# Performance work log

Hardware: AMD Instinct MI355X
Metric: run time of the kernel (lower is better)

Reference implementation:

```python
import jax, jax.numpy as jnp
import numpy as np

B, T, V, E, H = 1024, 256, 90, 8, 256


def setup_inputs() -> dict:
    key = jax.random.key(0)
    ks = jax.random.split(key, 40)
    rn = lambda k, shape: jax.random.normal(k, shape, dtype=jnp.float32) * 0.05
    inp = {}
    inp["input_seq"] = jax.random.randint(ks[0], (B, T), 0, V, dtype=jnp.int32)
    inp["emb"] = rn(ks[1], (V, E)).at[0].set(0.0)  # padding_idx=0
    i = 2
    for name, din in [("g1", E), ("g2", H), ("l1", E), ("l2", H)]:
        inp[name + "_Wih"] = rn(ks[i], (4 * H, din)); i += 1
        inp[name + "_Whh"] = rn(ks[i], (4 * H, H)); i += 1
        inp[name + "_bih"] = rn(ks[i], (4 * H,)); i += 1
        inp[name + "_bhh"] = rn(ks[i], (4 * H,)); i += 1
    for name in ["p1", "p2"]:
        inp[name + "_W1"] = rn(ks[i], (2 * H, E + 4 * H)); i += 1
        inp[name + "_b1"] = rn(ks[i], (2 * H,)); i += 1
        inp[name + "_W2"] = rn(ks[i], (H, 2 * H)); i += 1
        inp[name + "_b2"] = rn(ks[i], (H,)); i += 1
        inp[name + "_W3"] = rn(ks[i], (2, H)); i += 1
        inp[name + "_b3"] = rn(ks[i], (2,)); i += 1
    inp["gfc_W"] = rn(ks[i], (V, H)); i += 1
    inp["gfc_b"] = rn(ks[i], (V,)); i += 1
    inp["lfc_W"] = rn(ks[i], (V, H)); i += 1
    inp["lfc_b"] = rn(ks[i], (V,))
    return inp


def _cell(x, h, c, Wih, Whh, bih, bhh):
    # PyTorch LSTMCell: gate order i, f, g, o
    g = x @ Wih.T + h @ Whh.T + (bih + bhh)
    i, f, gg, o = jnp.split(g, 4, axis=-1)
    c = jax.nn.sigmoid(f) * c + jax.nn.sigmoid(i) * jnp.tanh(gg)
    return jax.nn.sigmoid(o) * jnp.tanh(c), c


def _mlp(x, W1, b1, W2, b2, W3, b3):
    h = jax.nn.relu(x @ W1.T + b1)
    h = jax.nn.relu(h @ W2.T + b2)
    return h @ W3.T + b3


def _forward(input_seq, emb,
             g1_Wih, g1_Whh, g1_bih, g1_bhh, g2_Wih, g2_Whh, g2_bih, g2_bhh,
             l1_Wih, l1_Whh, l1_bih, l1_bhh, l2_Wih, l2_Whh, l2_bih, l2_bhh,
             p1_W1, p1_b1, p1_W2, p1_b2, p1_W3, p1_b3,
             p2_W1, p2_b1, p2_W2, p2_b2, p2_W3, p2_b3,
             gfc_W, gfc_b, lfc_W, lfc_b):
    Bn = input_seq.shape[0]
    embeds = emb[input_seq]  # [B, T, E]
    z = jnp.zeros((Bn, H), dtype=emb.dtype)

    def step(carry, e):
        gh1, gc1, gh2, gc2, lh1, lc1, lh2, lc2 = carry
        gh1, gc1 = _cell(e, gh1, gc1, g1_Wih, g1_Whh, g1_bih, g1_bhh)
        lh1, lc1 = _cell(e, lh1, lc1, l1_Wih, l1_Whh, l1_bih, l1_bhh)
        p = jax.nn.softmax(_mlp(jnp.concatenate([e, gh1, gc1, lh1, lc1], 1),
                                p1_W1, p1_b1, p1_W2, p1_b2, p1_W3, p1_b3), axis=1)
        # bmm([B,1,2],[B,2,H]) == p0*local + p1*global
        gh1 = p[:, 0:1] * lh1 + p[:, 1:2] * gh1
        gc1 = p[:, 0:1] * lc1 + p[:, 1:2] * gc1
        gh2, gc2 = _cell(gh1, gh2, gc2, g2_Wih, g2_Whh, g2_bih, g2_bhh)
        lh2, lc2 = _cell(lh1, lh2, lc2, l2_Wih, l2_Whh, l2_bih, l2_bhh)
        p = jax.nn.softmax(_mlp(jnp.concatenate([e, gh2, gc2, lh2, lc2], 1),
                                p2_W1, p2_b1, p2_W2, p2_b2, p2_W3, p2_b3), axis=1)
        gh2 = p[:, 0:1] * lh2 + p[:, 1:2] * gh2
        gc2 = p[:, 0:1] * lc2 + p[:, 1:2] * gc2
        return (gh1, gc1, gh2, gc2, lh1, lc1, lh2, lc2), gh2

    _, hs = jax.lax.scan(step, (z, z, z, z, z, z, z, z), jnp.swapaxes(embeds, 0, 1))
    hs = jnp.swapaxes(hs, 0, 1)  # [B, T, H]
    out = 0.5 * (hs @ gfc_W.T + gfc_b) + 0.5 * (hs @ lfc_W.T + lfc_b)
    return jnp.swapaxes(out, 1, 2)  # [B, V, T]


def reference(input_seq, emb,
              g1_Wih, g1_Whh, g1_bih, g1_bhh, g2_Wih, g2_Whh, g2_bih, g2_bhh,
              l1_Wih, l1_Whh, l1_bih, l1_bhh, l2_Wih, l2_Whh, l2_bih, l2_bhh,
              p1_W1, p1_b1, p1_W2, p1_b2, p1_W3, p1_b3,
              p2_W1, p2_b1, p2_W2, p2_b2, p2_W3, p2_b3,
              gfc_W, gfc_b, lfc_W, lfc_b):
    return _forward(input_seq, emb,
                    g1_Wih, g1_Whh, g1_bih, g1_bhh, g2_Wih, g2_Whh, g2_bih, g2_bhh,
                    l1_Wih, l1_Whh, l1_bih, l1_bhh, l2_Wih, l2_Whh, l2_bih, l2_bhh,
                    p1_W1, p1_b1, p1_W2, p1_b2, p1_W3, p1_b3,
                    p2_W1, p2_b1, p2_W2, p2_b2, p2_W3, p2_b3,
                    gfc_W, gfc_b, lfc_W, lfc_b)
```

## Files before the change

kernel.cpp:

```cpp
#include <hip/hip_runtime.h>

#define B_ 1024
#define T_ 256
#define V_ 90
#define H_ 256
#define NTHR 512
#define NBLK 256
#define S_ ((size_t)B_*H_)

typedef unsigned short u16;
typedef __attribute__((ext_vector_type(8))) _Float16 f16x8;
typedef __attribute__((ext_vector_type(4))) _Float16 f16x4;
typedef __attribute__((ext_vector_type(4))) float f32x4;

constexpr size_t OFF_GH1C  = 0;
constexpr size_t OFF_GC1C  = OFF_GH1C + S_;
constexpr size_t OFF_GH1P  = OFF_GC1C + S_;
constexpr size_t OFF_GC1P  = OFF_GH1P + S_;
constexpr size_t OFF_LH1   = OFF_GC1P + S_;
constexpr size_t OFF_LC1   = OFF_LH1 + 2*S_;
constexpr size_t OFF_GH2C  = OFF_LC1 + 2*S_;
constexpr size_t OFF_GC2C  = OFF_GH2C + S_;
constexpr size_t OFF_GH2P  = OFF_GC2C + S_;
constexpr size_t OFF_GC2P  = OFF_GH2P + S_;
constexpr size_t OFF_LH2   = OFF_GC2P + S_;
constexpr size_t OFF_LC2   = OFF_LH2 + 2*S_;
constexpr size_t OFF_M1H   = OFF_LC2 + 2*S_;
constexpr size_t OFF_M2H   = OFF_M1H + (size_t)B_*512/2;
constexpr size_t OFF_OSTG  = OFF_M2H + (size_t)B_*512/2;
constexpr size_t OFF_EX    = OFF_OSTG + (size_t)B_*16*90;
constexpr size_t OFF_WG1PK = OFF_EX + 2*B_*8;
constexpr size_t OFF_WE1   = OFF_WG1PK + 256*2048/2;
constexpr size_t OFF_BG1   = OFF_WE1 + 8*2048;
constexpr size_t OFF_WL2PK = OFF_BG1 + 2048;
constexpr size_t OFF_BL2   = OFF_WL2PK + 512*1024/2;
constexpr size_t OFF_WG2PK = OFF_BL2 + 1024;
constexpr size_t OFF_BG2   = OFF_WG2PK + 512*1024/2;
constexpr size_t OFF_WP1PK = OFF_BG2 + 1024;
constexpr size_t OFF_WEP1  = OFF_WP1PK + 1024*512/2;
constexpr size_t OFF_WP2PK = OFF_WEP1 + 8*512;
constexpr size_t OFF_WEP2  = OFF_WP2PK + 1024*512/2;
constexpr size_t OFF_WB1   = OFF_WEP2 + 8*512;
constexpr size_t OFF_WB2   = OFF_WB1 + 512*256/2;
constexpr size_t OFF_WOUT  = OFF_WB2 + 512*256/2;
constexpr size_t OFF_BOUT  = OFF_WOUT + 256*96;
constexpr size_t OFF_BAR   = OFF_BOUT + 128;
constexpr size_t WS_FLOATS = OFF_BAR + 8192;

struct InP {
  const int*   seq;
  const float* emb;
  const float *g1_Wih,*g1_Whh,*g1_bih,*g1_bhh;
  const float *g2_Wih,*g2_Whh,*g2_bih,*g2_bhh;
  const float *l1_Wih,*l1_Whh,*l1_bih,*l1_bhh;
  const float *l2_Wih,*l2_Whh,*l2_bih,*l2_bhh;
  const float *p1_W1,*p1_b1,*p1_W2,*p1_b2,*p1_W3,*p1_b3;
  const float *p2_W1,*p2_b1,*p2_W2,*p2_b2,*p2_W3,*p2_b3;
  const float *gfc_W,*gfc_b,*lfc_W,*lfc_b;
};

__device__ __forceinline__ float sig_(float x)  { return 1.f/(1.f+__expf(-x)); }
__device__ __forceinline__ float tanh_(float x) { return 1.f - 2.f/(__expf(2.f*x)+1.f); }
__device__ __forceinline__ u16 f2h(float v) {
  _Float16 h = (_Float16)v; return __builtin_bit_cast(unsigned short, h);
}

__device__ __forceinline__ unsigned ld_flag(const unsigned* p) {
  unsigned v;
  asm volatile("global_load_dword %0, %1, off sc1\n\ts_waitcnt vmcnt(0)"
               : "=v"(v) : "v"(p) : "memory");
  return v;
}
__device__ __forceinline__ void st_flag(unsigned* p, unsigned v) {
  asm volatile("global_store_dword %0, %1, off sc1\n\ts_waitcnt vmcnt(0)"
               :: "v"(p), "v"(v) : "memory");
}

__device__ __forceinline__ void gbar_x(unsigned* arr, int slot, unsigned ep)
{
  __syncthreads();
  if (threadIdx.x == 0) st_flag(&arr[slot*16], ep);
  if (threadIdx.x < 32) {
    int cap = 0;
    for (;;) {
      unsigned v = ld_flag(&arr[threadIdx.x*16]);
      if (v >= ep) break;
      __builtin_amdgcn_s_sleep(1);
      if (++cap > 200000) break;
    }
  }
  __syncthreads();
  asm volatile("buffer_inv sc0" ::: "memory");
}

__device__ __forceinline__ void gl_lds16(const void* g, void* l) {
  __builtin_amdgcn_global_load_lds(
      (const __attribute__((address_space(1))) unsigned int*)g,
      (__attribute__((address_space(3))) unsigned int*)l, 16, 0, 2);
}
__device__ __forceinline__ void dma64(const u16* src) {
  extern __shared__ u16 dynB[];
  const int wv = threadIdx.x >> 6, lane = threadIdx.x & 63;
  const char* g = (const char*)src + lane*16;
  char* l = (char*)dynB;
#pragma unroll
  for (int j = 0; j < 8; ++j) {
    const int ofs = (wv*8 + j) * 1024;
    gl_lds16(g + ofs, l + ofs);
  }
}

template<int NCH, int NSEG, bool HASE, int TPW, class FE>
__device__ __forceinline__ void mm_lds(
    const float* s0, const float* s1_, const float* s2_, const float* s3_,
    const float* WeP, int ldwe, const float* ex,
    int rows0, int ct0, FE fe)
{
  extern __shared__ u16 dynB[];
  const int tid = threadIdx.x, lane = tid & 63, wr = tid >> 6;
  const int row = rows0 + wr*16 + (lane & 15);
  const int kq  = (lane >> 4) << 3;

  f32x4 acc[TPW];
#pragma unroll
  for (int t = 0; t < TPW; ++t) acc[t] = (f32x4){0,0,0,0};

  float4 alo[4], ahi[4];
  auto ldA = [&](int c, float4& lo, float4& hi) {
    const int k0 = c * 32;
    const float* S;
    if (NSEG == 1) S = s0;
    else if (NSEG == 2) S = (k0 < 256) ? s0 : s1_;
    else S = (k0 < 256) ? s0 : (k0 < 512) ? s1_ : (k0 < 768) ? s2_ : s3_;
    const float* p = &S[(size_t)row*H_ + (k0 & 255) + kq];
    lo = *(const float4*)p; hi = *(const float4*)(p + 4);
  };
  auto comp = [&](int c, const float4& lo, const float4& hi) {
    float av[8] = {lo.x,lo.y,lo.z,lo.w,hi.x,hi.y,hi.z,hi.w};
    f16x8 a;
#pragma unroll
    for (int j = 0; j < 8; ++j) a[j] = (_Float16)av[j];
#pragma unroll
    for (int t = 0; t < TPW; ++t) {
      f16x8 b = *(const f16x8*)(dynB + (size_t)(c*TPW + t)*512 + lane*8);
      acc[t] = __builtin_amdgcn_mfma_f32_16x16x32_f16(a, b, acc[t], 0, 0, 0);
    }
  };

#pragma unroll
  for (int c = 0; c < 4; ++c) ldA(c, alo[c], ahi[c]);
#pragma unroll
  for (int c = 0; c < NCH; ++c) {
    comp(c, alo[c & 3], ahi[c & 3]);
    if (c + 4 < NCH) ldA(c + 4, alo[c & 3], ahi[c & 3]);
  }

  if (HASE) {
#pragma unroll
    for (int t = 0; t < TPW; ++t) {
      const int colL = ct0 + t*16 + (lane & 15);
      float w[8];
#pragma unroll
      for (int j = 0; j < 8; ++j) w[j] = WeP[j*ldwe + colL];
#pragma unroll
      for (int m = 0; m < 4; ++m) {
        const int rr = rows0 + wr*16 + ((lane >> 4) << 2) + m;
        float s = 0.f;
#pragma unroll
        for (int j = 0; j < 8; ++j) s = __builtin_fmaf(ex[rr*8 + j], w[j], s);
        acc[t][m] += s;
      }
    }
  }
  fe(wr, lane, acc);
}

template<int TPW>
struct GateEpiM {
  const float* cin; float* ho; float* co; const float* bias_pk;
  int rows0; int ct0;
  __device__ void operator()(int wr, int lane, f32x4 (&acc)[TPW]) const {
    const int rbase = rows0 + wr*16 + ((lane >> 4) << 2);
#pragma unroll
    for (int gi = 0; gi < TPW/4; ++gi) {
      const int cb = ct0 + gi*64;
      const int h = (((cb & 1023) >> 6) << 4) + (lane & 15);
      float b[4];
#pragma unroll
      for (int t = 0; t < 4; ++t) b[t] = bias_pk[cb + t*16 + (lane & 15)];
#pragma unroll
      for (int m = 0; m < 4; ++m) {
        const size_t ix = (size_t)(rbase + m)*H_ + h;
        float gI = sig_(acc[gi*4+0][m] + b[0]);
        float gF = sig_(acc[gi*4+1][m] + b[1]);
        float gG = tanh_(acc[gi*4+2][m] + b[2]);
        float gO = sig_(acc[gi*4+3][m] + b[3]);
        float cn = gF*cin[ix] + gI*gG;
        ho[ix] = gO*tanh_(cn); co[ix] = cn;
      }
    }
  }
};

struct MlpEpiH {
  u16* dst; const float* b1; int rows0; int ct0;
  __device__ void operator()(int wr, int lane, f32x4 (&acc)[2]) const {
    const int rbase = rows0 + wr*16 + ((lane >> 4) << 2);
#pragma unroll
    for (int t = 0; t < 2; ++t) {
      const int c = ct0 + t*16 + (lane & 15);
      const float bb = b1[c];
#pragma unroll
      for (int m = 0; m < 4; ++m)
        dst[(size_t)(rbase + m)*512 + c] = f2h(fmaxf(acc[t][m] + bb, 0.f));
    }
  }
};

__device__ __forceinline__ void stage_F2(
    int rowbase,
    const u16* M, const u16* WBpk, const float* b2,
    const float* W3, const float* b3,
    const float* lh, const float* lc,
    const float* ghp, const float* gcp,
    float* ghc, float* gcc)
{
  const int w = threadIdx.x >> 6, lane = threadIdx.x & 63;
  const int r0 = rowbase + w*2;
  const u16* a0 = M + (size_t)r0*512;
  const u16* a1 = a0 + 512;
  float m0[4] = {0.f,0.f,0.f,0.f}, m1[4] = {0.f,0.f,0.f,0.f};
  for (int k0 = 0; k0 < 512; k0 += 4) {
    f16x4 x0 = *(const f16x4*)&a0[k0];
    f16x4 x1 = *(const f16x4*)&a1[k0];
#pragma unroll
    for (int j = 0; j < 4; ++j) {
      f16x4 wv = *(const f16x4*)&WBpk[(size_t)(k0+j)*256 + lane*4];
      float w0 = (float)wv[0], w1 = (float)wv[1], w2 = (float)wv[2], w3v = (float)wv[3];
      float xv0 = (float)x0[j], xv1 = (float)x1[j];
      m0[0] = __builtin_fmaf(xv0, w0, m0[0]);
      m0[1] = __builtin_fmaf(xv0, w1, m0[1]);
      m0[2] = __builtin_fmaf(xv0, w2, m0[2]);
      m0[3] = __builtin_fmaf(xv0, w3v, m0[3]);
      m1[0] = __builtin_fmaf(xv1, w0, m1[0]);
      m1[1] = __builtin_fmaf(xv1, w1, m1[1]);
      m1[2] = __builtin_fmaf(xv1, w2, m1[2]);
      m1[3] = __builtin_fmaf(xv1, w3v, m1[3]);
    }
  }
  float4 b = *(const float4*)&b2[lane*4];
  float bb2[4] = {b.x,b.y,b.z,b.w};
#pragma unroll
  for (int j = 0; j < 4; ++j) {
    m0[j] = fmaxf(m0[j]+bb2[j], 0.f);
    m1[j] = fmaxf(m1[j]+bb2[j], 0.f);
  }
  float4 w30 = *(const float4*)&W3[lane*4];
  float4 w31 = *(const float4*)&W3[256 + lane*4];
  float w0v[4] = {w30.x,w30.y,w30.z,w30.w};
  float w1v[4] = {w31.x,w31.y,w31.z,w31.w};
  float d00=0.f, d01=0.f, d10=0.f, d11=0.f;
#pragma unroll
  for (int j = 0; j < 4; ++j) {
    d00 = __builtin_fmaf(m0[j], w0v[j], d00);
    d01 = __builtin_fmaf(m0[j], w1v[j], d01);
    d10 = __builtin_fmaf(m1[j], w0v[j], d10);
    d11 = __builtin_fmaf(m1[j], w1v[j], d11);
  }
#pragma unroll
  for (int off = 32; off; off >>= 1) {
    d00 += __shfl_xor(d00, off, 64); d01 += __shfl_xor(d01, off, 64);
    d10 += __shfl_xor(d10, off, 64); d11 += __shfl_xor(d11, off, 64);
  }
  d00 += b3[0]; d01 += b3[1]; d10 += b3[0]; d11 += b3[1];
  float mxa = fmaxf(d00, d01), mxb = fmaxf(d10, d11);
  float e00 = __expf(d00-mxa), e01 = __expf(d01-mxa);
  float e10 = __expf(d10-mxb), e11 = __expf(d11-mxb);
  float ia = 1.f/(e00+e01), ib = 1.f/(e10+e11);
  float p0a = e00*ia, p1a = e01*ia;
  float p0b = e10*ib, p1b = e11*ib;
#pragma unroll
  for (int rr = 0; rr < 2; ++rr) {
    const float p0 = rr ? p0b : p0a, p1 = rr ? p1b : p1a;
    const size_t ix = (size_t)(r0+rr)*H_ + lane*4;
    float4 lv = *(const float4*)&lh[ix];
    float4 gv = *(const float4*)&ghp[ix];
    float4 o;
    o.x = p0*lv.x + p1*gv.x; o.y = p0*lv.y + p1*gv.y;
    o.z = p0*lv.z + p1*gv.z; o.w = p0*lv.w + p1*gv.w;
    *(float4*)&ghc[ix] = o;
    lv = *(const float4*)&lc[ix];
    gv = *(const float4*)&gcp[ix];
    o.x = p0*lv.x + p1*gv.x; o.y = p0*lv.y + p1*gv.y;
    o.z = p0*lv.z + p1*gv.z; o.w = p0*lv.w + p1*gv.w;
    *(float4*)&gcc[ix] = o;
  }
}

__device__ __forceinline__ void stage_OUTS(
    const float* gh2c, const float* WOUT, const float* BOUT,
    float* ostg, int rbase, int tt)
{
  const int w = threadIdx.x >> 6, lane = threadIdx.x & 63;
  const bool two = lane < (V_ - 64);
#pragma unroll
  for (int rr = 0; rr < 2; ++rr) {
    const int r = rbase + w*2 + rr;
    const float* arow = gh2c + (size_t)r * H_;
    float acc0 = 0.f, acc1 = 0.f;
    for (int k0 = 0; k0 < 256; k0 += 4) {
      float4 a4 = *(const float4*)&arow[k0];
      float av[4] = {a4.x, a4.y, a4.z, a4.w};
#pragma unroll
      for (int j = 0; j < 4; ++j) {
        const float* wr_ = &WOUT[(size_t)(k0+j)*96];
        acc0 = __builtin_fmaf(av[j], wr_[lane], acc0);
        if (two) acc1 = __builtin_fmaf(av[j], wr_[64+lane], acc1);
      }
    }
    float* dst = &ostg[((size_t)r*16 + (tt & 15))*90];
    if (lane < 64) dst[lane] = acc0 + BOUT[lane];
    if (two) dst[64+lane] = acc1 + BOUT[64+lane];
  }
}

__device__ __forceinline__ void flush_out(
    const float* ostg, float* out, int rbase, int tb0)
{
  for (int i = threadIdx.x; i < 16*90; i += NTHR) {
    const int rr = i / 90, v = i - rr*90;
    const int r = rbase + rr;
    const float* src = &ostg[((size_t)r*16)*90 + v];
    float tmp[16];
#pragma unroll
    for (int tb = 0; tb < 16; ++tb) tmp[tb] = src[tb*90];
    float* dst = &out[((size_t)r*V_ + v)*T_ + tb0];
#pragma unroll
    for (int q = 0; q < 4; ++q)
      ((float4*)dst)[q] = make_float4(tmp[q*4], tmp[q*4+1], tmp[q*4+2], tmp[q*4+3]);
  }
}

__global__ void k_setup(InP in, float* __restrict__ ws)
{
  const size_t nthr = (size_t)gridDim.x * blockDim.x;
  const size_t t0 = (size_t)blockIdx.x * blockDim.x + threadIdx.x;

  for (size_t i = t0; i < 16*S_; i += nthr) ws[i] = 0.f;
  for (size_t i = t0; i < 8192; i += nthr) ((unsigned*)(ws + OFF_BAR))[i] = 0u;

  for (size_t i = t0; i < (size_t)B_*8; i += nthr) {
    int r = (int)(i >> 3), j = (int)(i & 7);
    ws[OFF_EX + i] = in.emb[(size_t)in.seq[(size_t)r*T_]*8 + j];
  }

  {
    u16* dst = (u16*)(ws + OFF_WG1PK);
    for (size_t i = t0; i < (size_t)16*8*8*512; i += nthr) {
      int e = (int)(i & 7), lane = (int)((i >> 3) & 63);
      int tile = (int)((i >> 9) & 7), ck = (int)((i >> 12) & 7), blk = (int)(i >> 15);
      int col = blk*128 + tile*16 + (lane & 15);
      int k = ck*32 + ((lane >> 4) << 3) + e;
      int cell = col >> 10, q = col & 1023;
      int h = ((q >> 6) << 4) + (q & 15), g = (q >> 4) & 3, R = g*256 + h;
      dst[i] = f2h((cell ? in.l1_Whh : in.g1_Whh)[(size_t)R*256 + k]);
    }
  }
  for (size_t i = t0; i < (size_t)8*2048; i += nthr) {
    int j = (int)(i >> 11), p = (int)(i & 2047);
    int cell = p >> 10, q = p & 1023;
    int h = ((q >> 6) << 4) + (q & 15), g = (q >> 4) & 3, R = g*256 + h;
    ws[OFF_WE1 + (size_t)j*2048 + p] = (cell ? in.l1_Wih : in.g1_Wih)[(size_t)R*8 + j];
  }
  for (size_t i = t0; i < 2048; i += nthr) {
    int p = (int)i, cell = p >> 10, q = p & 1023;
    int h = ((q >> 6) << 4) + (q & 15), g = (q >> 4) & 3, R = g*256 + h;
    ws[OFF_BG1 + i] = cell ? (in.l1_bih[R] + in.l1_bhh[R]) : (in.g1_bih[R] + in.g1_bhh[R]);
  }

  for (int which = 0; which < 2; ++which) {
    u16* dst = (u16*)(ws + (which ? OFF_WG2PK : OFF_WL2PK));
    const float* Wih = which ? in.g2_Wih : in.l2_Wih;
    const float* Whh = which ? in.g2_Whh : in.l2_Whh;
    for (size_t i = t0; i < (size_t)16*16*4*512; i += nthr) {
      int e = (int)(i & 7), lane = (int)((i >> 3) & 63);
      int tile = (int)((i >> 9) & 3), ck = (int)((i >> 11) & 15), blk = (int)(i >> 15);
      int col = blk*64 + tile*16 + (lane & 15);
      int k = ck*32 + ((lane >> 4) << 3) + e;
      int h = ((col >> 6) << 4) + (col & 15), g = (col >> 4) & 3, R = g*256 + h;
      float w = (k < 256) ? Wih[(size_t)R*256 + k] : Whh[(size_t)R*256 + (k-256)];
      dst[i] = f2h(w);
    }
  }
  for (size_t i = t0; i < 2*1024; i += nthr) {
    int which = (int)(i >> 10), p = (int)(i & 1023);
    int h = ((p >> 6) << 4) + (p & 15), g = (p >> 4) & 3, R = g*256 + h;
    float v = which ? (in.g2_bih[R] + in.g2_bhh[R]) : (in.l2_bih[R] + in.l2_bhh[R]);
    ws[(which ? OFF_BG2 : OFF_BL2) + p] = v;
  }

  for (int which = 0; which < 2; ++which) {
    u16* dst = (u16*)(ws + (which ? OFF_WP2PK : OFF_WP1PK));
    const float* W = which ? in.p2_W1 : in.p1_W1;
    for (size_t i = t0; i < (size_t)16*32*2*512; i += nthr) {
      int e = (int)(i & 7), lane = (int)((i >> 3) & 63);
      int tile = (int)((i >> 9) & 1), ck = (int)((i >> 10) & 31), blk = (int)(i >> 15);
      int col = blk*32 + tile*16 + (lane & 15);
      int k = ck*32 + ((lane >> 4) << 3) + e;
      dst[i] = f2h(W[(size_t)col*1032 + 8 + k]);
    }
  }
  for (size_t i = t0; i < (size_t)2*8*512; i += nthr) {
    int which = (int)(i / (8*512));
    int idx = (int)(i - (size_t)which*8*512);
    int j = idx >> 9, p = idx & 511;
    const float* W = which ? in.p2_W1 : in.p1_W1;
    ws[(which ? OFF_WEP2 : OFF_WEP1) + (size_t)j*512 + p] = W[(size_t)p*1032 + j];
  }

  for (size_t i = t0; i < (size_t)2*512*256; i += nthr) {
    int which = (int)(i / (512*256));
    int idx = (int)(i - (size_t)which*512*256);
    int k = idx >> 8, n = idx & 255;
    const float* W = which ? in.p2_W2 : in.p1_W2;
    ((u16*)(ws + (which ? OFF_WB2 : OFF_WB1)))[idx] = f2h(W[(size_t)n*512 + k]);
  }
  for (size_t i = t0; i < (size_t)256*96; i += nthr) {
    int k = (int)(i / 96), c = (int)(i - (size_t)k*96);
    float v = 0.f;
    if (c < V_) v = 0.5f*(in.gfc_W[(size_t)c*256 + k] + in.lfc_W[(size_t)c*256 + k]);
    ws[OFF_WOUT + i] = v;
  }
  for (size_t i = t0; i < 96; i += nthr)
    ws[OFF_BOUT + i] = (i < V_) ? 0.5f*(in.gfc_b[i] + in.lfc_b[i]) : 0.f;
}

__global__ __launch_bounds__(NTHR) void k_main(InP in, float* ws, float* __restrict__ out)
{
  __shared__ __attribute__((aligned(16))) volatile float s_pad[6144];
  __shared__ unsigned s_slot;

  float* GH1C = ws + OFF_GH1C;  float* GC1C = ws + OFF_GC1C;
  float* GH1P = ws + OFF_GH1P;  float* GC1P = ws + OFF_GC1P;
  float* LH1  = ws + OFF_LH1;   float* LC1  = ws + OFF_LC1;
  float* GH2C = ws + OFF_GH2C;  float* GC2C = ws + OFF_GC2C;
  float* GH2P = ws + OFF_GH2P;  float* GC2P = ws + OFF_GC2P;
  float* LH2  = ws + OFF_LH2;   float* LC2  = ws + OFF_LC2;
  u16*   M1H  = (u16*)(ws + OFF_M1H);
  u16*   M2H  = (u16*)(ws + OFF_M2H);
  float* OSTG = ws + OFF_OSTG;
  float* EXB  = ws + OFF_EX;
  const u16* WG1PK = (const u16*)(ws + OFF_WG1PK);
  const u16* WL2PK = (const u16*)(ws + OFF_WL2PK);
  const u16* WG2PK = (const u16*)(ws + OFF_WG2PK);
  const u16* WP1PK = (const u16*)(ws + OFF_WP1PK);
  const u16* WP2PK = (const u16*)(ws + OFF_WP2PK);
  const u16* WB1PK = (const u16*)(ws + OFF_WB1);
  const u16* WB2PK = (const u16*)(ws + OFF_WB2);
  const float* WE1  = ws + OFF_WE1;  const float* BG1P = ws + OFF_BG1;
  const float* BL2P = ws + OFF_BL2;  const float* BG2P = ws + OFF_BG2;
  const float* WEP1 = ws + OFF_WEP1; const float* WEP2 = ws + OFF_WEP2;
  const float* WOUT = ws + OFF_WOUT; const float* BOUT = ws + OFF_BOUT;

  unsigned xcc;
  asm volatile("s_getreg_b32 %0, hwreg(HW_REG_XCC_ID)" : "=s"(xcc));
  xcc &= 7u;
  unsigned* barx = ((unsigned*)(ws + OFF_BAR)) + xcc*1024;
  unsigned* arr  = barx;
  unsigned* reg  = barx + 544;
  if (threadIdx.x == 0) {
    s_slot = __hip_atomic_fetch_add(reg, 1u, __ATOMIC_RELAXED, __HIP_MEMORY_SCOPE_AGENT);
    s_pad[0] = (float)s_slot;
  }
  __syncthreads();
  const int slot  = (int)(s_slot & 31u);
  const int rows0 = (int)xcc * 128;
  const int s2 = slot & 15;
  unsigned ep = 0;

  if (slot < 16) dma64(WG1PK + (size_t)slot*32768);
  else           dma64(WG2PK + (size_t)s2*32768);
  asm volatile("s_waitcnt vmcnt(0)" ::: "memory");
  __syncthreads();

  for (int n = 0; n <= T_; ++n) {
    const int sel = n & 1;
    const float* ex  = EXB + sel*(B_*8);
    const float* exm = EXB + (sel^1)*(B_*8);
    float* lh1o = LH1 + sel*S_;   float* lh1n = LH1 + (sel^1)*S_;
    float* lc1o = LC1 + sel*S_;   float* lc1n = LC1 + (sel^1)*S_;
    float* lh2o = LH2 + sel*S_;   float* lh2n = LH2 + (sel^1)*S_;
    float* lc2o = LC2 + sel*S_;   float* lc2n = LC2 + (sel^1)*S_;

    if (slot < 16) {
      if (n < T_) {
        const int ct0 = slot*128;
        const int cell = slot >> 3;
        GateEpiM<8> epi{ cell ? lc1o : GC1C,
                         cell ? lh1n : GH1P,
                         cell ? lc1n : GC1P,
                         BG1P, rows0, ct0 };
        mm_lds<8,1,true,8>(cell ? lh1o : GH1C, nullptr, nullptr, nullptr,
                           WE1, 2048, ex, rows0, ct0, epi);
      }
    } else if (n >= 1) {
      const int ct0 = s2*64;
      GateEpiM<4> epi{ GC2C, GH2P, GC2P, BG2P, rows0, ct0 };
      mm_lds<16,2,false,4>(GH1C, GH2C, nullptr, nullptr,
                           nullptr, 0, nullptr, rows0, ct0, epi);
    }
    __syncthreads();
    {
      if (slot < 16) dma64(WP1PK + (size_t)s2*32768);
      else           dma64(WP2PK + (size_t)s2*32768);
    }
    gbar_x(arr, slot, ++ep);

    if (slot < 16) {
      if (n < T_) {
        const int ct0 = s2*32;
        MlpEpiH epi{ M1H, in.p1_b1, rows0, ct0 };
        mm_lds<32,4,true,2>(GH1P, GC1P, lh1n, lc1n,
                            WEP1, 512, ex, rows0, ct0, epi);
      }
    } else if (n >= 1) {
      const int ct0 = s2*32;
      MlpEpiH epi{ M2H, in.p2_b1, rows0, ct0 };
      mm_lds<32,4,true,2>(GH2P, GC2P, lh2o, lc2o,
                          WEP2, 512, exm, rows0, ct0, epi);
    }
    __syncthreads();
    if (n < T_) {
      if (slot < 16) dma64(WL2PK + (size_t)slot*32768);
      else           dma64(WG2PK + (size_t)s2*32768);
    }
    gbar_x(arr, slot, ++ep);

    if (slot < 16) {
      if (n < T_) {
        const int ct0 = slot*64;
        GateEpiM<4> epi{ lc2o, lh2n, lc2n, BL2P, rows0, ct0 };
        mm_lds<16,2,false,4>(lh1n, lh2o, nullptr, nullptr,
                             nullptr, 0, nullptr, rows0, ct0, epi);
      }
    } else if (slot < 24) {
      if (n < T_) {
        const int rb = rows0 + (slot-16)*16;
        stage_F2(rb, M1H, WB1PK, in.p1_b2, in.p1_W3, in.p1_b3,
                 lh1n, lc1n, GH1P, GC1P, GH1C, GC1C);
        if (n + 1 < T_ && threadIdx.x < 128) {
          const int r = rb + (threadIdx.x >> 3), j = threadIdx.x & 7;
          EXB[(sel^1)*(B_*8) + r*8 + j] =
              in.emb[(size_t)in.seq[(size_t)r*T_ + n + 1]*8 + j];
        }
      }
    } else {
      if (n >= 1) {
        const int rb = rows0 + (slot-24)*16;
        stage_F2(rb, M2H, WB2PK, in.p2_b2, in.p2_W3, in.p2_b3,
                 lh2o, lc2o, GH2P, GC2P, GH2C, GC2C);
        __syncthreads();
        stage_OUTS(GH2C, WOUT, BOUT, OSTG, rb, n-1);
        if (((n-1) & 15) == 15) {
          __syncthreads();
          flush_out(OSTG, out, rb, n-16);
        }
      }
    }
    __syncthreads();
    if (n < T_ - 1) {
      if (slot < 16) dma64(WG1PK + (size_t)slot*32768);
    }
    gbar_x(arr, slot, ++ep);
  }
}

extern "C" void kernel_launch(void* const* d_in, const int* in_sizes, int n_in,
                              void* d_out, int out_size, void* d_ws, size_t ws_size,
                              hipStream_t stream)
{
  if (ws_size < WS_FLOATS * sizeof(float)) return;

  InP in;
  in.seq    = (const int*)  d_in[0];
  in.emb    = (const float*)d_in[1];
  in.g1_Wih = (const float*)d_in[2];  in.g1_Whh = (const float*)d_in[3];
  in.g1_bih = (const float*)d_in[4];  in.g1_bhh = (const float*)d_in[5];
  in.g2_Wih = (const float*)d_in[6];  in.g2_Whh = (const float*)d_in[7];
  in.g2_bih = (const float*)d_in[8];  in.g2_bhh = (const float*)d_in[9];
  in.l1_Wih = (const float*)d_in[10]; in.l1_Whh = (const float*)d_in[11];
  in.l1_bih = (const float*)d_in[12]; in.l1_bhh = (const float*)d_in[13];
  in.l2_Wih = (const float*)d_in[14]; in.l2_Whh = (const float*)d_in[15];
  in.l2_bih = (const float*)d_in[16]; in.l2_bhh = (const float*)d_in[17];
  in.p1_W1  = (const float*)d_in[18]; in.p1_b1  = (const float*)d_in[19];
  in.p1_W2  = (const float*)d_in[20]; in.p1_b2  = (const float*)d_in[21];
  in.p1_W3  = (const float*)d_in[22]; in.p1_b3  = (const float*)d_in[23];
  in.p2_W1  = (const float*)d_in[24]; in.p2_b1  = (const float*)d_in[25];
  in.p2_W2  = (const float*)d_in[26]; in.p2_b2  = (const float*)d_in[27];
  in.p2_W3  = (const float*)d_in[28]; in.p2_b3  = (const float*)d_in[29];
  in.gfc_W  = (const float*)d_in[30]; in.gfc_b  = (const float*)d_in[31];
  in.lfc_W  = (const float*)d_in[32]; in.lfc_b  = (const float*)d_in[33];

  float* ws  = (float*)d_ws;
  float* out = (float*)d_out;

  k_setup<<<512, 256, 0, stream>>>(in, ws);
  k_main <<<NBLK, NTHR, 65536, stream>>>(in, ws, out);
}
```

Before: 57.61 ms.

## Double-buffer LDS weight tiles and store hidden states in fp16

```diff
diff --git a/kernel.cpp b/kernel.cpp
--- a/kernel.cpp
+++ b/kernel.cpp
@@ -7,6 +7,7 @@
 #define NTHR 512
 #define NBLK 256
 #define S_ ((size_t)B_*H_)
+#define HS_ (S_/2)
 
 typedef unsigned short u16;
 typedef __attribute__((ext_vector_type(8))) _Float16 f16x8;
@@ -14,17 +15,21 @@
 typedef __attribute__((ext_vector_type(4))) float f32x4;
 
 constexpr size_t OFF_GH1C  = 0;
-constexpr size_t OFF_GC1C  = OFF_GH1C + S_;
-constexpr size_t OFF_GH1P  = OFF_GC1C + S_;
-constexpr size_t OFF_GC1P  = OFF_GH1P + S_;
-constexpr size_t OFF_LH1   = OFF_GC1P + S_;
-constexpr size_t OFF_LC1   = OFF_LH1 + 2*S_;
-constexpr size_t OFF_GH2C  = OFF_LC1 + 2*S_;
-constexpr size_t OFF_GC2C  = OFF_GH2C + S_;
-constexpr size_t OFF_GH2P  = OFF_GC2C + S_;
-constexpr size_t OFF_GC2P  = OFF_GH2P + S_;
-constexpr size_t OFF_LH2   = OFF_GC2P + S_;
-constexpr size_t OFF_LC2   = OFF_LH2 + 2*S_;
+constexpr size_t OFF_GH1P  = OFF_GH1C + HS_;
+constexpr size_t OFF_LH1   = OFF_GH1P + HS_;
+constexpr size_t OFF_GH2C  = OFF_LH1 + 2*HS_;
+constexpr size_t OFF_GH2P  = OFF_GH2C + HS_;
+constexpr size_t OFF_LH2   = OFF_GH2P + HS_;
+constexpr size_t OFF_GC1PH = OFF_LH2 + 2*HS_;
+constexpr size_t OFF_LC1H  = OFF_GC1PH + HS_;
+constexpr size_t OFF_GC2PH = OFF_LC1H + 2*HS_;
+constexpr size_t OFF_LC2H  = OFF_GC2PH + HS_;
+constexpr size_t OFF_GC1C  = OFF_LC2H + 2*HS_;
+constexpr size_t OFF_GC1P  = OFF_GC1C + S_;
+constexpr size_t OFF_LC1   = OFF_GC1P + S_;
+constexpr size_t OFF_GC2C  = OFF_LC1 + 2*S_;
+constexpr size_t OFF_GC2P  = OFF_GC2C + S_;
+constexpr size_t OFF_LC2   = OFF_GC2P + S_;
 constexpr size_t OFF_M1H   = OFF_LC2 + 2*S_;
 constexpr size_t OFF_M2H   = OFF_M1H + (size_t)B_*512/2;
 constexpr size_t OFF_OSTG  = OFF_M2H + (size_t)B_*512/2;
@@ -98,11 +103,10 @@
       (const __attribute__((address_space(1))) unsigned int*)g,
       (__attribute__((address_space(3))) unsigned int*)l, 16, 0, 2);
 }
-__device__ __forceinline__ void dma64(const u16* src) {
-  extern __shared__ u16 dynB[];
+__device__ __forceinline__ void dma64(const u16* src, u16* dstbase) {
   const int wv = threadIdx.x >> 6, lane = threadIdx.x & 63;
   const char* g = (const char*)src + lane*16;
-  char* l = (char*)dynB;
+  char* l = (char*)dstbase;
 #pragma unroll
   for (int j = 0; j < 8; ++j) {
     const int ofs = (wv*8 + j) * 1024;
@@ -112,11 +116,11 @@
 
 template<int NCH, int NSEG, bool HASE, int TPW, class FE>
 __device__ __forceinline__ void mm_lds(
-    const float* s0, const float* s1_, const float* s2_, const float* s3_,
+    const u16* bufp,
+    const u16* s0, const u16* s1_, const u16* s2_, const u16* s3_,
     const float* WeP, int ldwe, const float* ex,
     int rows0, int ct0, FE fe)
 {
-  extern __shared__ u16 dynB[];
   const int tid = threadIdx.x, lane = tid & 63, wr = tid >> 6;
   const int row = rows0 + wr*16 + (lane & 15);
   const int kq  = (lane >> 4) << 3;
@@ -125,34 +129,28 @@
 #pragma unroll
   for (int t = 0; t < TPW; ++t) acc[t] = (f32x4){0,0,0,0};
 
-  float4 alo[4], ahi[4];
-  auto ldA = [&](int c, float4& lo, float4& hi) {
+  constexpr int DEP = (NCH < 8) ? NCH : 8;
+  f16x8 areg[DEP];
+  auto ldA = [&](int c) -> f16x8 {
     const int k0 = c * 32;
-    const float* S;
+    const u16* S;
     if (NSEG == 1) S = s0;
     else if (NSEG == 2) S = (k0 < 256) ? s0 : s1_;
     else S = (k0 < 256) ? s0 : (k0 < 512) ? s1_ : (k0 < 768) ? s2_ : s3_;
-    const float* p = &S[(size_t)row*H_ + (k0 & 255) + kq];
-    lo = *(const float4*)p; hi = *(const float4*)(p + 4);
+    return *(const f16x8*)&S[(size_t)row*H_ + (k0 & 255) + kq];
   };
-  auto comp = [&](int c, const float4& lo, const float4& hi) {
-    float av[8] = {lo.x,lo.y,lo.z,lo.w,hi.x,hi.y,hi.z,hi.w};
-    f16x8 a;
-#pragma unroll
-    for (int j = 0; j < 8; ++j) a[j] = (_Float16)av[j];
+
+#pragma unroll
+  for (int c = 0; c < DEP; ++c) areg[c] = ldA(c);
+#pragma unroll
+  for (int c = 0; c < NCH; ++c) {
+    f16x8 a = areg[c % DEP];
 #pragma unroll
     for (int t = 0; t < TPW; ++t) {
-      f16x8 b = *(const f16x8*)(dynB + (size_t)(c*TPW + t)*512 + lane*8);
+      f16x8 b = *(const f16x8*)(bufp + (size_t)(c*TPW + t)*512 + lane*8);
       acc[t] = __builtin_amdgcn_mfma_f32_16x16x32_f16(a, b, acc[t], 0, 0, 0);
     }
-  };
-
-#pragma unroll
-  for (int c = 0; c < 4; ++c) ldA(c, alo[c], ahi[c]);
-#pragma unroll
-  for (int c = 0; c < NCH; ++c) {
-    comp(c, alo[c & 3], ahi[c & 3]);
-    if (c + 4 < NCH) ldA(c + 4, alo[c & 3], ahi[c & 3]);
+    if (c + DEP < NCH) areg[c % DEP] = ldA(c + DEP);
   }
 
   if (HASE) {
@@ -177,7 +175,7 @@
 
 template<int TPW>
 struct GateEpiM {
-  const float* cin; float* ho; float* co; const float* bias_pk;
+  const float* cin; u16* ho; float* co; u16* coh; const float* bias_pk;
   int rows0; int ct0;
   __device__ void operator()(int wr, int lane, f32x4 (&acc)[TPW]) const {
     const int rbase = rows0 + wr*16 + ((lane >> 4) << 2);
@@ -196,7 +194,9 @@
         float gG = tanh_(acc[gi*4+2][m] + b[2]);
         float gO = sig_(acc[gi*4+3][m] + b[3]);
         float cn = gF*cin[ix] + gI*gG;
-        ho[ix] = gO*tanh_(cn); co[ix] = cn;
+        ho[ix] = f2h(gO*tanh_(cn));
+        co[ix] = cn;
+        coh[ix] = f2h(cn);
       }
     }
   }
@@ -221,9 +221,9 @@
     int rowbase,
     const u16* M, const u16* WBpk, const float* b2,
     const float* W3, const float* b3,
-    const float* lh, const float* lc,
-    const float* ghp, const float* gcp,
-    float* ghc, float* gcc)
+    const u16* lh, const float* lc,
+    const u16* ghp, const float* gcp,
+    u16* ghc, float* gcc)
 {
   const int w = threadIdx.x >> 6, lane = threadIdx.x & 63;
   const int r0 = rowbase + w*2;
@@ -283,22 +283,24 @@
   for (int rr = 0; rr < 2; ++rr) {
     const float p0 = rr ? p0b : p0a, p1 = rr ? p1b : p1a;
     const size_t ix = (size_t)(r0+rr)*H_ + lane*4;
-    float4 lv = *(const float4*)&lh[ix];
-    float4 gv = *(const float4*)&ghp[ix];
-    float4 o;
-    o.x = p0*lv.x + p1*gv.x; o.y = p0*lv.y + p1*gv.y;
-    o.z = p0*lv.z + p1*gv.z; o.w = p0*lv.w + p1*gv.w;
-    *(float4*)&ghc[ix] = o;
-    lv = *(const float4*)&lc[ix];
-    gv = *(const float4*)&gcp[ix];
-    o.x = p0*lv.x + p1*gv.x; o.y = p0*lv.y + p1*gv.y;
-    o.z = p0*lv.z + p1*gv.z; o.w = p0*lv.w + p1*gv.w;
-    *(float4*)&gcc[ix] = o;
+    f16x4 lv = *(const f16x4*)&lh[ix];
+    f16x4 gv = *(const f16x4*)&ghp[ix];
+    f16x4 oh;
+#pragma unroll
+    for (int j = 0; j < 4; ++j)
+      oh[j] = (_Float16)(p0*(float)lv[j] + p1*(float)gv[j]);
+    *(f16x4*)&ghc[ix] = oh;
+    float4 lcv = *(const float4*)&lc[ix];
+    float4 gcv = *(const float4*)&gcp[ix];
+    float4 oc;
+    oc.x = p0*lcv.x + p1*gcv.x; oc.y = p0*lcv.y + p1*gcv.y;
+    oc.z = p0*lcv.z + p1*gcv.z; oc.w = p0*lcv.w + p1*gcv.w;
+    *(float4*)&gcc[ix] = oc;
   }
 }
 
 __device__ __forceinline__ void stage_OUTS(
-    const float* gh2c, const float* WOUT, const float* BOUT,
+    const u16* gh2c, const float* WOUT, const float* BOUT,
     float* ostg, int rbase, int tt)
 {
   const int w = threadIdx.x >> 6, lane = threadIdx.x & 63;
@@ -306,20 +308,20 @@
 #pragma unroll
   for (int rr = 0; rr < 2; ++rr) {
     const int r = rbase + w*2 + rr;
-    const float* arow = gh2c + (size_t)r * H_;
+    const u16* arow = gh2c + (size_t)r * H_;
     float acc0 = 0.f, acc1 = 0.f;
-    for (int k0 = 0; k0 < 256; k0 += 4) {
-      float4 a4 = *(const float4*)&arow[k0];
-      float av[4] = {a4.x, a4.y, a4.z, a4.w};
-#pragma unroll
-      for (int j = 0; j < 4; ++j) {
+    for (int k0 = 0; k0 < 256; k0 += 8) {
+      f16x8 a8 = *(const f16x8*)&arow[k0];
+#pragma unroll
+      for (int j = 0; j < 8; ++j) {
+        const float av = (float)a8[j];
         const float* wr_ = &WOUT[(size_t)(k0+j)*96];
-        acc0 = __builtin_fmaf(av[j], wr_[lane], acc0);
-        if (two) acc1 = __builtin_fmaf(av[j], wr_[64+lane], acc1);
+        acc0 = __builtin_fmaf(av, wr_[lane], acc0);
+        if (two) acc1 = __builtin_fmaf(av, wr_[64+lane], acc1);
       }
     }
     float* dst = &ostg[((size_t)r*16 + (tt & 15))*90];
-    if (lane < 64) dst[lane] = acc0 + BOUT[lane];
+    dst[lane] = acc0 + BOUT[lane];
     if (two) dst[64+lane] = acc1 + BOUT[64+lane];
   }
 }
@@ -346,7 +348,7 @@
   const size_t nthr = (size_t)gridDim.x * blockDim.x;
   const size_t t0 = (size_t)blockIdx.x * blockDim.x + threadIdx.x;
 
-  for (size_t i = t0; i < 16*S_; i += nthr) ws[i] = 0.f;
+  for (size_t i = t0; i < OFF_M1H; i += nthr) ws[i] = 0.f;
   for (size_t i = t0; i < 8192; i += nthr) ((unsigned*)(ws + OFF_BAR))[i] = 0u;
 
   for (size_t i = t0; i < (size_t)B_*8; i += nthr) {
@@ -437,15 +439,24 @@
 
 __global__ __launch_bounds__(NTHR) void k_main(InP in, float* ws, float* __restrict__ out)
 {
-  __shared__ __attribute__((aligned(16))) volatile float s_pad[6144];
+  __shared__ __attribute__((aligned(16))) u16 sB0[32768];
+  extern __shared__ u16 dynB[];
   __shared__ unsigned s_slot;
 
-  float* GH1C = ws + OFF_GH1C;  float* GC1C = ws + OFF_GC1C;
-  float* GH1P = ws + OFF_GH1P;  float* GC1P = ws + OFF_GC1P;
-  float* LH1  = ws + OFF_LH1;   float* LC1  = ws + OFF_LC1;
-  float* GH2C = ws + OFF_GH2C;  float* GC2C = ws + OFF_GC2C;
-  float* GH2P = ws + OFF_GH2P;  float* GC2P = ws + OFF_GC2P;
-  float* LH2  = ws + OFF_LH2;   float* LC2  = ws + OFF_LC2;
+  u16*  GH1C = (u16*)(ws + OFF_GH1C);
+  u16*  GH1P = (u16*)(ws + OFF_GH1P);
+  u16*  LH1  = (u16*)(ws + OFF_LH1);
+  u16*  GH2C = (u16*)(ws + OFF_GH2C);
+  u16*  GH2P = (u16*)(ws + OFF_GH2P);
+  u16*  LH2  = (u16*)(ws + OFF_LH2);
+  u16*  GC1PH= (u16*)(ws + OFF_GC1PH);
+  u16*  LC1H = (u16*)(ws + OFF_LC1H);
+  u16*  GC2PH= (u16*)(ws + OFF_GC2PH);
+  u16*  LC2H = (u16*)(ws + OFF_LC2H);
+  float* GC1C = ws + OFF_GC1C;  float* GC1P = ws + OFF_GC1P;
+  float* LC1  = ws + OFF_LC1;
+  float* GC2C = ws + OFF_GC2C;  float* GC2P = ws + OFF_GC2P;
+  float* LC2  = ws + OFF_LC2;
   u16*   M1H  = (u16*)(ws + OFF_M1H);
   u16*   M2H  = (u16*)(ws + OFF_M2H);
   float* OSTG = ws + OFF_OSTG;
@@ -468,18 +479,17 @@
   unsigned* barx = ((unsigned*)(ws + OFF_BAR)) + xcc*1024;
   unsigned* arr  = barx;
   unsigned* reg  = barx + 544;
-  if (threadIdx.x == 0) {
+  if (threadIdx.x == 0)
     s_slot = __hip_atomic_fetch_add(reg, 1u, __ATOMIC_RELAXED, __HIP_MEMORY_SCOPE_AGENT);
-    s_pad[0] = (float)s_slot;
-  }
   __syncthreads();
   const int slot  = (int)(s_slot & 31u);
   const int rows0 = (int)xcc * 128;
   const int s2 = slot & 15;
   unsigned ep = 0;
-
-  if (slot < 16) dma64(WG1PK + (size_t)slot*32768);
-  else           dma64(WG2PK + (size_t)s2*32768);
+  int wb = 0;
+
+  if (slot < 16) dma64(WG1PK + (size_t)slot*32768, sB0);
+  else           dma64(WG2PK + (size_t)s2*32768, sB0);
   asm volatile("s_waitcnt vmcnt(0)" ::: "memory");
   __syncthreads();
 
@@ -487,11 +497,18 @@
     const int sel = n & 1;
     const float* ex  = EXB + sel*(B_*8);
     const float* exm = EXB + (sel^1)*(B_*8);
-    float* lh1o = LH1 + sel*S_;   float* lh1n = LH1 + (sel^1)*S_;
-    float* lc1o = LC1 + sel*S_;   float* lc1n = LC1 + (sel^1)*S_;
-    float* lh2o = LH2 + sel*S_;   float* lh2n = LH2 + (sel^1)*S_;
-    float* lc2o = LC2 + sel*S_;   float* lc2n = LC2 + (sel^1)*S_;
-
+    u16* lh1o = LH1 + sel*(B_*H_);   u16* lh1n = LH1 + (sel^1)*(B_*H_);
+    float* lc1o = LC1 + sel*S_;      float* lc1n = LC1 + (sel^1)*S_;
+    u16* lc1nh = LC1H + (sel^1)*(B_*H_);
+    u16* lh2o = LH2 + sel*(B_*H_);   u16* lh2n = LH2 + (sel^1)*(B_*H_);
+    float* lc2o = LC2 + sel*S_;      float* lc2n = LC2 + (sel^1)*S_;
+    u16* lc2oh = LC2H + sel*(B_*H_); u16* lc2nh = LC2H + (sel^1)*(B_*H_);
+
+    u16* bC; u16* bF;
+
+    bC = wb ? dynB : sB0; bF = wb ? sB0 : dynB;
+    if (slot < 16) dma64(WP1PK + (size_t)s2*32768, bF);
+    else           dma64(WP2PK + (size_t)s2*32768, bF);
     if (slot < 16) {
       if (n < T_) {
         const int ct0 = slot*128;
@@ -499,48 +516,46 @@
         GateEpiM<8> epi{ cell ? lc1o : GC1C,
                          cell ? lh1n : GH1P,
                          cell ? lc1n : GC1P,
+                         cell ? lc1nh : GC1PH,
                          BG1P, rows0, ct0 };
-        mm_lds<8,1,true,8>(cell ? lh1o : GH1C, nullptr, nullptr, nullptr,
+        mm_lds<8,1,true,8>(bC, cell ? lh1o : GH1C, nullptr, nullptr, nullptr,
                            WE1, 2048, ex, rows0, ct0, epi);
       }
     } else if (n >= 1) {
       const int ct0 = s2*64;
-      GateEpiM<4> epi{ GC2C, GH2P, GC2P, BG2P, rows0, ct0 };
-      mm_lds<16,2,false,4>(GH1C, GH2C, nullptr, nullptr,
+      GateEpiM<4> epi{ GC2C, GH2P, GC2P, GC2PH, BG2P, rows0, ct0 };
+      mm_lds<16,2,false,4>(bC, GH1C, GH2C, nullptr, nullptr,
                            nullptr, 0, nullptr, rows0, ct0, epi);
     }
-    __syncthreads();
-    {
-      if (slot < 16) dma64(WP1PK + (size_t)s2*32768);
-      else           dma64(WP2PK + (size_t)s2*32768);
-    }
     gbar_x(arr, slot, ++ep);
-
+    wb ^= 1;
+
+    bC = wb ? dynB : sB0; bF = wb ? sB0 : dynB;
+    if (slot < 16) dma64(WL2PK + (size_t)slot*32768, bF);
+    else           dma64(WG2PK + (size_t)s2*32768, bF);
     if (slot < 16) {
       if (n < T_) {
         const int ct0 = s2*32;
         MlpEpiH epi{ M1H, in.p1_b1, rows0, ct0 };
-        mm_lds<32,4,true,2>(GH1P, GC1P, lh1n, lc1n,
+        mm_lds<32,4,true,2>(bC, GH1P, GC1PH, lh1n, lc1nh,
                             WEP1, 512, ex, rows0, ct0, epi);
       }
     } else if (n >= 1) {
       const int ct0 = s2*32;
       MlpEpiH epi{ M2H, in.p2_b1, rows0, ct0 };
-      mm_lds<32,4,true,2>(GH2P, GC2P, lh2o, lc2o,
+      mm_lds<32,4,true,2>(bC, GH2P, GC2PH, lh2o, lc2oh,
                           WEP2, 512, exm, rows0, ct0, epi);
     }
-    __syncthreads();
-    if (n < T_) {
-      if (slot < 16) dma64(WL2PK + (size_t)slot*32768);
-      else           dma64(WG2PK + (size_t)s2*32768);
-    }
     gbar_x(arr, slot, ++ep);
-
+    wb ^= 1;
+
+    bC = wb ? dynB : sB0; bF = wb ? sB0 : dynB;
     if (slot < 16) {
+      dma64(WG1PK + (size_t)slot*32768, bF);
       if (n < T_) {
         const int ct0 = slot*64;
-        GateEpiM<4> epi{ lc2o, lh2n, lc2n, BL2P, rows0, ct0 };
-        mm_lds<16,2,false,4>(lh1n, lh2o, nullptr, nullptr,
+        GateEpiM<4> epi{ lc2o, lh2n, lc2n, lc2nh, BL2P, rows0, ct0 };
+        mm_lds<16,2,false,4>(bC, lh1n, lh2o, nullptr, nullptr,
                              nullptr, 0, nullptr, rows0, ct0, epi);
       }
     } else if (slot < 24) {
@@ -567,11 +582,8 @@
         }
       }
     }
-    __syncthreads();
-    if (n < T_ - 1) {
-      if (slot < 16) dma64(WG1PK + (size_t)slot*32768);
-    }
     gbar_x(arr, slot, ++ep);
+    if (slot < 16) wb ^= 1;
   }
 }
 
```

New measurement: 56.92 ms. Within noise of the previous version (-1.2%).
